# Performance work log

Hardware: AMD Instinct MI355X
Metric: run time of the kernel (lower is better)

The kernel has to match this reference:

```python
import jax, jax.numpy as jnp
import numpy as np


def setup_inputs() -> dict:
    key = jax.random.key(0)
    kx, kv, kw, kb = jax.random.split(key, 4)
    B, D, A = 16384, 4096, 21
    x = jax.random.normal(kx, (B, D), dtype=jnp.float32)
    v = jax.random.normal(kv, (B, A), dtype=jnp.float32)
    # Stacked per-annotator Linear(dim,1) weights/biases: W[A, D], b[A]
    W = jax.random.normal(kw, (A, D), dtype=jnp.float32) * (1.0 / np.sqrt(D))
    b = jax.random.normal(kb, (A,), dtype=jnp.float32) * 0.01
    return {"x": x, "v": v, "W": W, "b": b}


def reference(x, v, W, b):
    # Fused form of 21 parallel Linear(dim,1) heads (dropout p=0 is identity):
    # out[b, a] = x[b, :] @ W[a, :] + b[a]
    out = jnp.einsum("bd,ad->ba", x, W) + b  # [B, A]
    result = jnp.sum(out * v, axis=1)          # [B]
    return (result, out)
```

## Files before the change

### kernel.cpp

```cpp
#include <hip/hip_runtime.h>
#include <hip/hip_bf16.h>

#define DDIM 4096
#define ADIM 21
#define BM   64
#define KC   128
#define NCH  (DDIM / KC)
#define NTHR 256

typedef __attribute__((ext_vector_type(8))) short bf16x8;
typedef __attribute__((ext_vector_type(4))) float f32x4;

#define XOFF(b) ((b) * 16384)
#define WOFF(b) (32768 + (b) * 8192)

__device__ __forceinline__ int swz(int row, int kbyte) {
    return (row * 256 + kbyte) ^ ((row & 7) << 4);
}

__device__ __forceinline__ unsigned pk2(float lo, float hi) {
    unsigned short a = __builtin_bit_cast(unsigned short, __float2bfloat16(lo));
    unsigned short b = __builtin_bit_cast(unsigned short, __float2bfloat16(hi));
    return (unsigned)a | ((unsigned)b << 16);
}

__global__ __launch_bounds__(NTHR, 1)
void fem_mfma(const float* __restrict__ x,
              const float* __restrict__ v,
              const float* __restrict__ W,
              const float* __restrict__ bias,
              float* __restrict__ result,
              float* __restrict__ out)
{
    __shared__ char smem[49152];
    const int t = threadIdx.x;
    const int rowbase = blockIdx.x * BM;

    float4 xA[8], xB[8], wA[4], wB[4];

    auto issue = [&](int c, float4 xr[8], float4 wr[4]) {
        const float* xs = x + (size_t)(rowbase + (t >> 4)) * DDIM + c * KC + (t & 15) * 8;
#pragma unroll
        for (int j = 0; j < 4; ++j) {
            const float* s = xs + (size_t)j * 16 * DDIM;
            xr[2 * j]     = *(const float4*)s;
            xr[2 * j + 1] = *(const float4*)(s + 4);
        }
        const float* ws = W + (size_t)(t >> 4) * DDIM + c * KC + (t & 15) * 8;
        wr[0] = *(const float4*)ws;
        wr[1] = *(const float4*)(ws + 4);
        if (t < 80) {
            const float* w2 = W + (size_t)(16 + (t >> 4)) * DDIM + c * KC + (t & 15) * 8;
            wr[2] = *(const float4*)w2;
            wr[3] = *(const float4*)(w2 + 4);
        }
    };

    auto write_stage = [&](int buf, const float4 xr[8], const float4 wr[4]) {
        char* xb = smem + XOFF(buf);
        const int kg = t & 15;
#pragma unroll
        for (int j = 0; j < 4; ++j) {
            const int row = (t >> 4) + j * 16;
            uint4 g;
            g.x = pk2(xr[2 * j].x, xr[2 * j].y);
            g.y = pk2(xr[2 * j].z, xr[2 * j].w);
            g.z = pk2(xr[2 * j + 1].x, xr[2 * j + 1].y);
            g.w = pk2(xr[2 * j + 1].z, xr[2 * j + 1].w);
            *(uint4*)(xb + swz(row, kg * 16)) = g;
        }
        char* wb = smem + WOFF(buf);
        {
            uint4 g;
            g.x = pk2(wr[0].x, wr[0].y); g.y = pk2(wr[0].z, wr[0].w);
            g.z = pk2(wr[1].x, wr[1].y); g.w = pk2(wr[1].z, wr[1].w);
            *(uint4*)(wb + swz(t >> 4, kg * 16)) = g;
        }
        if (t < 80) {
            uint4 g;
            g.x = pk2(wr[2].x, wr[2].y); g.y = pk2(wr[2].z, wr[2].w);
            g.z = pk2(wr[3].x, wr[3].y); g.w = pk2(wr[3].z, wr[3].w);
            *(uint4*)(wb + swz(16 + (t >> 4), kg * 16)) = g;
        }
    };

    const int lane = t & 63;
    const int wv   = t >> 6;
    const int a0   = lane & 15;
    const int kh   = (lane >> 4) * 8;
    const int rA   = wv * 16 + a0 - a0 + (lane & 15);

    f32x4 acc0, acc1;
    {
        const float ba0 = bias[a0];
        const float ba1 = (a0 < 5) ? bias[16 + a0] : 0.f;
        acc0 = (f32x4){ba0, ba0, ba0, ba0};
        acc1 = (f32x4){ba1, ba1, ba1, ba1};
    }

    auto compute = [&](int buf) {
        const char* xb = smem + XOFF(buf);
        const char* wb = smem + WOFF(buf);
        const int rowA = wv * 16 + (lane & 15);
#pragma unroll
        for (int k0 = 0; k0 < KC; k0 += 32) {
            bf16x8 a  = *(const bf16x8*)(xb + swz(rowA,        (k0 + kh) * 2));
            bf16x8 b0 = *(const bf16x8*)(wb + swz(a0,          (k0 + kh) * 2));
            bf16x8 b1 = *(const bf16x8*)(wb + swz(16 + a0,     (k0 + kh) * 2));
            acc0 = __builtin_amdgcn_mfma_f32_16x16x32_bf16(a, b0, acc0, 0, 0, 0);
            acc1 = __builtin_amdgcn_mfma_f32_16x16x32_bf16(a, b1, acc1, 0, 0, 0);
        }
    };

    if (t < 176) {
        const int row = 21 + (t >> 4), kg = t & 15;
        const uint4 z = {0, 0, 0, 0};
        *(uint4*)(smem + WOFF(0) + swz(row, kg * 16)) = z;
        *(uint4*)(smem + WOFF(1) + swz(row, kg * 16)) = z;
    }
    issue(0, xA, wA);
    write_stage(0, xA, wA);
    issue(1, xB, wB);
    __syncthreads();

    for (int c = 0; c < NCH; c += 2) {
        if (c + 2 < NCH) issue(c + 2, xA, wA);
        compute(0);
        __syncthreads();
        write_stage(1, xB, wB);
        if (c + 3 < NCH) issue(c + 3, xB, wB);
        __syncthreads();
        compute(1);
        __syncthreads();
        if (c + 2 < NCH) write_stage(0, xA, wA);
        __syncthreads();
    }

    const size_t growbase = (size_t)rowbase + wv * 16 + (lane >> 4) * 4;
#pragma unroll
    for (int r = 0; r < 4; ++r) {
        const size_t row = growbase + r;
        float o0 = acc0[r];
        out[row * ADIM + a0] = o0;
        float p = o0 * v[row * ADIM + a0];
        if (a0 < 5) {
            float o1 = acc1[r];
            out[row * ADIM + 16 + a0] = o1;
            p += o1 * v[row * ADIM + 16 + a0];
        }
        p += __shfl_xor(p, 1);
        p += __shfl_xor(p, 2);
        p += __shfl_xor(p, 4);
        p += __shfl_xor(p, 8);
        if (a0 == 0) result[row] = p;
    }
}

extern "C" void kernel_launch(void* const* d_in, const int* in_sizes, int n_in,
                              void* d_out, int out_size, void* d_ws, size_t ws_size,
                              hipStream_t stream) {
    const float* x  = (const float*)d_in[0];
    const float* v  = (const float*)d_in[1];
    const float* W  = (const float*)d_in[2];
    const float* b  = (const float*)d_in[3];

    const int B = in_sizes[0] / DDIM;

    float* result = (float*)d_out;
    float* out    = (float*)d_out + B;

    fem_mfma<<<dim3(B / BM), dim3(NTHR), 0, stream>>>(x, v, W, b, result, out);
}
```

Before: 55.21 us.

## Split K dimension across two blocks with atomic accumulation

Splits the 4096-wide reduction into two halves, each handled by a separate block along grid y, and combines partial outputs with atomicAdd after zeroing the output via hipMemsetAsync. Launch bounds now allow two blocks per CU. This doubles the grid (256 to 512 blocks) so more CUs and waves are busy hiding memory latency. In exchange it adds a memset, atomic traffic, and nondeterministic float summation order.

```diff
diff --git a/kernel.cpp b/kernel.cpp
--- a/kernel.cpp
+++ b/kernel.cpp
@@ -5,7 +5,7 @@
 #define ADIM 21
 #define BM   64
 #define KC   128
-#define NCH  (DDIM / KC)
+#define NCHH 16
 #define NTHR 256
 
 typedef __attribute__((ext_vector_type(8))) short bf16x8;
@@ -24,7 +24,7 @@
     return (unsigned)a | ((unsigned)b << 16);
 }
 
-__global__ __launch_bounds__(NTHR, 1)
+__global__ __launch_bounds__(NTHR, 2)
 void fem_mfma(const float* __restrict__ x,
               const float* __restrict__ v,
               const float* __restrict__ W,
@@ -35,6 +35,7 @@
     __shared__ char smem[49152];
     const int t = threadIdx.x;
     const int rowbase = blockIdx.x * BM;
+    const int cb = blockIdx.y * NCHH;
 
     float4 xA[8], xB[8], wA[4], wB[4];
 
@@ -88,14 +89,16 @@
     const int wv   = t >> 6;
     const int a0   = lane & 15;
     const int kh   = (lane >> 4) * 8;
-    const int rA   = wv * 16 + a0 - a0 + (lane & 15);
 
     f32x4 acc0, acc1;
-    {
+    if (blockIdx.y == 0) {
         const float ba0 = bias[a0];
         const float ba1 = (a0 < 5) ? bias[16 + a0] : 0.f;
         acc0 = (f32x4){ba0, ba0, ba0, ba0};
         acc1 = (f32x4){ba1, ba1, ba1, ba1};
+    } else {
+        acc0 = (f32x4){0.f, 0.f, 0.f, 0.f};
+        acc1 = (f32x4){0.f, 0.f, 0.f, 0.f};
     }
 
     auto compute = [&](int buf) {
@@ -104,9 +107,9 @@
         const int rowA = wv * 16 + (lane & 15);
 #pragma unroll
         for (int k0 = 0; k0 < KC; k0 += 32) {
-            bf16x8 a  = *(const bf16x8*)(xb + swz(rowA,        (k0 + kh) * 2));
-            bf16x8 b0 = *(const bf16x8*)(wb + swz(a0,          (k0 + kh) * 2));
-            bf16x8 b1 = *(const bf16x8*)(wb + swz(16 + a0,     (k0 + kh) * 2));
+            bf16x8 a  = *(const bf16x8*)(xb + swz(rowA,    (k0 + kh) * 2));
+            bf16x8 b0 = *(const bf16x8*)(wb + swz(a0,      (k0 + kh) * 2));
+            bf16x8 b1 = *(const bf16x8*)(wb + swz(16 + a0, (k0 + kh) * 2));
             acc0 = __builtin_amdgcn_mfma_f32_16x16x32_bf16(a, b0, acc0, 0, 0, 0);
             acc1 = __builtin_amdgcn_mfma_f32_16x16x32_bf16(a, b1, acc1, 0, 0, 0);
         }
@@ -118,21 +121,21 @@
         *(uint4*)(smem + WOFF(0) + swz(row, kg * 16)) = z;
         *(uint4*)(smem + WOFF(1) + swz(row, kg * 16)) = z;
     }
-    issue(0, xA, wA);
+    issue(cb + 0, xA, wA);
     write_stage(0, xA, wA);
-    issue(1, xB, wB);
+    issue(cb + 1, xB, wB);
     __syncthreads();
 
-    for (int c = 0; c < NCH; c += 2) {
-        if (c + 2 < NCH) issue(c + 2, xA, wA);
+    for (int c = 0; c < NCHH; c += 2) {
+        if (c + 2 < NCHH) issue(cb + c + 2, xA, wA);
         compute(0);
         __syncthreads();
         write_stage(1, xB, wB);
-        if (c + 3 < NCH) issue(c + 3, xB, wB);
+        if (c + 3 < NCHH) issue(cb + c + 3, xB, wB);
         __syncthreads();
         compute(1);
         __syncthreads();
-        if (c + 2 < NCH) write_stage(0, xA, wA);
+        if (c + 2 < NCHH) write_stage(0, xA, wA);
         __syncthreads();
     }
 
@@ -141,18 +144,18 @@
     for (int r = 0; r < 4; ++r) {
         const size_t row = growbase + r;
         float o0 = acc0[r];
-        out[row * ADIM + a0] = o0;
+        atomicAdd(&out[row * ADIM + a0], o0);
         float p = o0 * v[row * ADIM + a0];
         if (a0 < 5) {
             float o1 = acc1[r];
-            out[row * ADIM + 16 + a0] = o1;
+            atomicAdd(&out[row * ADIM + 16 + a0], o1);
             p += o1 * v[row * ADIM + 16 + a0];
         }
         p += __shfl_xor(p, 1);
         p += __shfl_xor(p, 2);
         p += __shfl_xor(p, 4);
         p += __shfl_xor(p, 8);
-        if (a0 == 0) result[row] = p;
+        if (a0 == 0) atomicAdd(&result[row], p);
     }
 }
 
@@ -169,5 +172,7 @@
     float* result = (float*)d_out;
     float* out    = (float*)d_out + B;
 
-    fem_mfma<<<dim3(B / BM), dim3(NTHR), 0, stream>>>(x, v, W, b, result, out);
+    hipMemsetAsync(d_out, 0, (size_t)out_size * sizeof(float), stream);
+
+    fem_mfma<<<dim3(B / BM, 2), dim3(NTHR), 0, stream>>>(x, v, W, b, result, out);
 }
```

Result: slower. 56.32 us (+2.0%).

## Overlap LDS stage writes with MFMA compute and use lightweight barriers

Applied to the files above, without the earlier changes.

The double-buffered loop now writes the next LDS stage while the current stage is being computed. This halves the barriers per two chunks from four to two, and the prologue and epilogue are restructured to match. `__syncthreads` is replaced by a custom barrier that waits only on LDS counters (lgkmcnt), so global prefetches stay in flight across barriers instead of being drained. The kernel already streams x at close to HBM bandwidth, so the remaining room for improvement is small. The custom barrier depends on correct manual waitcnt handling.

```diff
diff --git a/kernel.cpp b/kernel.cpp
--- a/kernel.cpp
+++ b/kernel.cpp
@@ -36,9 +36,9 @@
     const int t = threadIdx.x;
     const int rowbase = blockIdx.x * BM;
 
-    float4 xA[8], xB[8], wA[4], wB[4];
+    float4 xE[8], xO[8], wE[4], wO[4];
 
-    auto issue = [&](int c, float4 xr[8], float4 wr[4]) {
+    auto issue = [&](int c, float4 (&xr)[8], float4 (&wr)[4]) {
         const float* xs = x + (size_t)(rowbase + (t >> 4)) * DDIM + c * KC + (t & 15) * 8;
 #pragma unroll
         for (int j = 0; j < 4; ++j) {
@@ -56,7 +56,7 @@
         }
     };
 
-    auto write_stage = [&](int buf, const float4 xr[8], const float4 wr[4]) {
+    auto write_stage = [&](int buf, const float4 (&xr)[8], const float4 (&wr)[4]) {
         char* xb = smem + XOFF(buf);
         const int kg = t & 15;
 #pragma unroll
@@ -88,7 +88,6 @@
     const int wv   = t >> 6;
     const int a0   = lane & 15;
     const int kh   = (lane >> 4) * 8;
-    const int rA   = wv * 16 + a0 - a0 + (lane & 15);
 
     f32x4 acc0, acc1;
     {
@@ -104,12 +103,18 @@
         const int rowA = wv * 16 + (lane & 15);
 #pragma unroll
         for (int k0 = 0; k0 < KC; k0 += 32) {
-            bf16x8 a  = *(const bf16x8*)(xb + swz(rowA,        (k0 + kh) * 2));
-            bf16x8 b0 = *(const bf16x8*)(wb + swz(a0,          (k0 + kh) * 2));
-            bf16x8 b1 = *(const bf16x8*)(wb + swz(16 + a0,     (k0 + kh) * 2));
+            bf16x8 a  = *(const bf16x8*)(xb + swz(rowA,    (k0 + kh) * 2));
+            bf16x8 b0 = *(const bf16x8*)(wb + swz(a0,      (k0 + kh) * 2));
+            bf16x8 b1 = *(const bf16x8*)(wb + swz(16 + a0, (k0 + kh) * 2));
             acc0 = __builtin_amdgcn_mfma_f32_16x16x32_bf16(a, b0, acc0, 0, 0, 0);
             acc1 = __builtin_amdgcn_mfma_f32_16x16x32_bf16(a, b1, acc1, 0, 0, 0);
         }
+    };
+
+    auto barrier = [&]() {
+        asm volatile("s_waitcnt lgkmcnt(0)" ::: "memory");
+        __builtin_amdgcn_s_barrier();
+        __builtin_amdgcn_sched_barrier(0);
     };
 
     if (t < 176) {
@@ -118,33 +123,36 @@
         *(uint4*)(smem + WOFF(0) + swz(row, kg * 16)) = z;
         *(uint4*)(smem + WOFF(1) + swz(row, kg * 16)) = z;
     }
-    issue(0, xA, wA);
-    write_stage(0, xA, wA);
-    issue(1, xB, wB);
-    __syncthreads();
+    issue(0, xE, wE);
+    issue(1, xO, wO);
+    write_stage(0, xE, wE);
+    issue(2, xE, wE);
+    barrier();
 
-    for (int c = 0; c < NCH; c += 2) {
-        if (c + 2 < NCH) issue(c + 2, xA, wA);
+    for (int c = 0; c <= NCH - 4; c += 2) {
+        write_stage(1, xO, wO);
+        issue(c + 3, xO, wO);
         compute(0);
-        __syncthreads();
-        write_stage(1, xB, wB);
-        if (c + 3 < NCH) issue(c + 3, xB, wB);
-        __syncthreads();
+        barrier();
+        write_stage(0, xE, wE);
+        if (c + 4 < NCH) issue(c + 4, xE, wE);
         compute(1);
-        __syncthreads();
-        if (c + 2 < NCH) write_stage(0, xA, wA);
-        __syncthreads();
+        barrier();
     }
+    write_stage(1, xO, wO);
+    compute(0);
+    barrier();
+    compute(1);
 
     const size_t growbase = (size_t)rowbase + wv * 16 + (lane >> 4) * 4;
 #pragma unroll
     for (int r = 0; r < 4; ++r) {
         const size_t row = growbase + r;
-        float o0 = acc0[r];
+        const float o0 = acc0[r];
         out[row * ADIM + a0] = o0;
         float p = o0 * v[row * ADIM + a0];
         if (a0 < 5) {
-            float o1 = acc1[r];
+            const float o1 = acc1[r];
             out[row * ADIM + 16 + a0] = o1;
             p += o1 * v[row * ADIM + 16 + a0];
         }
```

Result: no change. 56.18 us, median of 2 (+1.8%).
